# Performance work log

Measured on AMD Instinct MI355X. Metric: run time of the kernel, lower is better.

The kernel has to match this reference:

```python
import jax, jax.numpy as jnp
import numpy as np

B, S, H, NH = 4, 2048, 1024, 16
HD = H // NH
SCALE = 1.0 / np.sqrt(HD)
MASK_VAL = -1e9  # fp32 branch of the torch code


def setup_inputs() -> dict:
    key = jax.random.key(0)
    ks = jax.random.split(key, 6)
    s = 1.0 / np.sqrt(H)
    return {
        "x": jax.random.normal(ks[0], (B, S, H), dtype=jnp.float32),
        "attention_mask": jnp.ones((B, S), dtype=jnp.int32),
        "Wq": jax.random.normal(ks[1], (H, H), dtype=jnp.float32) * s,
        "Wk": jax.random.normal(ks[2], (H, H), dtype=jnp.float32) * s,
        "Wv": jax.random.normal(ks[3], (H, H), dtype=jnp.float32) * s,
        "Wo": jax.random.normal(ks[4], (H, H), dtype=jnp.float32) * s,
        "bo": jnp.zeros((H,), dtype=jnp.float32),
    }


def reference(x, attention_mask, Wq, Wk, Wv, Wo, bo):
    b, s, h = x.shape
    # projections; torch Linear computes x @ W.T
    q = (x @ Wq.T).reshape(b, s, NH, HD).transpose(0, 2, 1, 3)  # [b,nh,s,hd]
    k = (x @ Wk.T).reshape(b, s, NH, HD).transpose(0, 2, 1, 3)
    v = (x @ Wv.T).reshape(b, s, NH, HD).transpose(0, 2, 1, 3)

    scores = jnp.einsum("bhqd,bhkd->bhqk", q, k) * SCALE  # [b,nh,s,s]
    # padding mask: [b,1,1,s]
    pad = (attention_mask == 0)[:, None, None, :]
    scores = jnp.where(pad, MASK_VAL, scores)
    # causal mask
    causal = jnp.tril(jnp.ones((s, s), dtype=bool))[None, None]
    scores = jnp.where(causal, scores, MASK_VAL)

    attn = jax.nn.softmax(scores, axis=-1)  # dropout p=0 / eval -> identity
    out = jnp.einsum("bhqk,bhkd->bhqd", attn, v)
    out = out.transpose(0, 2, 1, 3).reshape(b, s, h)
    return out @ Wo.T + bo
```

## Files before the change

kernel.cpp:

```cpp
#include <hip/hip_runtime.h>

#define B_ 4
#define S_ 2048
#define H_ 1024
#define NH_ 16
#define HD_ 64
#define QSCALE_ 0.1803368801111204f

typedef __attribute__((ext_vector_type(8))) short bf16x8;
typedef __attribute__((ext_vector_type(4))) float f32x4;
typedef __attribute__((ext_vector_type(16))) float f32x16;

__device__ __forceinline__ unsigned short f2bf(float f) {
    unsigned u = __float_as_uint(f);
    unsigned r = (u + 0x7FFFu + ((u >> 16) & 1u)) >> 16;
    return (unsigned short)r;
}
__device__ __forceinline__ float exp2f_hw(float x) { return __builtin_amdgcn_exp2f(x); }

__global__ __launch_bounds__(256) void cast_all(const float* __restrict__ x,
                                                const float* __restrict__ Wq,
                                                const float* __restrict__ Wk,
                                                const float* __restrict__ Wv,
                                                const float* __restrict__ Wo,
                                                unsigned short* __restrict__ xb,
                                                unsigned short* __restrict__ Wqb,
                                                unsigned short* __restrict__ Wkb,
                                                unsigned short* __restrict__ Wvb,
                                                unsigned short* __restrict__ Wob) {
    int bid = blockIdx.x;
    const float* src;
    unsigned short* dst;
    int i;
    if (bid < 8192) {
        src = x; dst = xb; i = bid * 256 + threadIdx.x;
    } else {
        int k = bid - 8192, wsel = k >> 10;
        src = wsel == 0 ? Wq : wsel == 1 ? Wk : wsel == 2 ? Wv : Wo;
        dst = wsel == 0 ? Wqb : wsel == 1 ? Wkb : wsel == 2 ? Wvb : Wob;
        i = (k & 1023) * 256 + threadIdx.x;
    }
    float4 v = reinterpret_cast<const float4*>(src)[i];
    ushort4 o;
    o.x = f2bf(v.x); o.y = f2bf(v.y); o.z = f2bf(v.z); o.w = f2bf(v.w);
    reinterpret_cast<ushort4*>(dst)[i] = o;
}

__device__ __forceinline__ void stage128_swz(const char* g, int gstride, char* lds, int tid) {
    int wave = tid >> 6, lane = tid & 63;
#pragma unroll
    for (int j = 0; j < 4; ++j) {
        int o = ((wave * 4 + j) * 64 + lane) * 16;
        int r = o >> 7;
        int slot = (o >> 4) & 7;
        const char* src = g + (size_t)r * gstride + ((slot ^ (r & 7)) << 4);
        __builtin_amdgcn_global_load_lds((const __attribute__((address_space(1))) void*)src,
                                         (__attribute__((address_space(3))) void*)(lds + (wave * 4 + j) * 1024),
                                         16, 0, 0);
    }
}
__device__ __forceinline__ void stage64_swz(const char* g, int gstride, char* lds, int tid) {
    int wave = tid >> 6, lane = tid & 63;
#pragma unroll
    for (int j = 0; j < 2; ++j) {
        int o = ((wave * 2 + j) * 64 + lane) * 16;
        int r = o >> 7;
        int slot = (o >> 4) & 7;
        const char* src = g + (size_t)r * gstride + ((slot ^ (r & 7)) << 4);
        __builtin_amdgcn_global_load_lds((const __attribute__((address_space(1))) void*)src,
                                         (__attribute__((address_space(3))) void*)(lds + (wave * 2 + j) * 1024),
                                         16, 0, 0);
    }
}

__device__ __forceinline__ bf16x8 frag_swz(const char* lds, int row, int slot) {
    return *reinterpret_cast<const bf16x8*>(lds + row * 128 + (((slot) ^ (row & 7)) << 4));
}

__device__ __forceinline__ float vmax16(const f32x16& v) {
    float a0 = fmaxf(v[0], v[1]), a1 = fmaxf(v[2], v[3]);
    float a2 = fmaxf(v[4], v[5]), a3 = fmaxf(v[6], v[7]);
    float a4 = fmaxf(v[8], v[9]), a5 = fmaxf(v[10], v[11]);
    float a6 = fmaxf(v[12], v[13]), a7 = fmaxf(v[14], v[15]);
    float b0 = fmaxf(a0, a1), b1 = fmaxf(a2, a3), b2 = fmaxf(a4, a5), b3 = fmaxf(a6, a7);
    return fmaxf(fmaxf(b0, b1), fmaxf(b2, b3));
}

__global__ __launch_bounds__(256) void gemm_qkv(const unsigned short* __restrict__ xb,
                                                const unsigned short* __restrict__ Wq,
                                                const unsigned short* __restrict__ Wk,
                                                const unsigned short* __restrict__ Wv,
                                                unsigned short* __restrict__ Qo,
                                                unsigned short* __restrict__ Ko,
                                                unsigned short* __restrict__ Vo) {
    __shared__ __align__(16) char As[128 * 128];
    __shared__ __align__(16) char Bs[128 * 128];
    int tid = threadIdx.x, lane = tid & 63, wave = tid >> 6;
    int wr = wave >> 1, wc = wave & 1;
    int brow = blockIdx.x * 128;
    int mat = blockIdx.y >> 3;
    int bcol = (blockIdx.y & 7) * 128;
    const unsigned short* W = mat == 0 ? Wq : (mat == 1 ? Wk : Wv);
    unsigned short* O = mat == 0 ? Qo : (mat == 1 ? Ko : Vo);
    float oscale = (mat == 0) ? QSCALE_ : 1.0f;
    f32x4 acc[4][4] = {};
    const char* ga = (const char*)(xb + (size_t)brow * H_);
    const char* gb = (const char*)(W + (size_t)bcol * H_);
    int ro = lane & 15, kg = lane >> 4;
    for (int kt = 0; kt < H_ / 64; ++kt) {
        stage128_swz(ga + kt * 128, H_ * 2, As, tid);
        stage128_swz(gb + kt * 128, H_ * 2, Bs, tid);
        __syncthreads();
#pragma unroll
        for (int kk = 0; kk < 2; ++kk) {
            bf16x8 af[4], bfr[4];
#pragma unroll
            for (int m = 0; m < 4; ++m) af[m] = frag_swz(As, wr * 64 + m * 16 + ro, kk * 4 + kg);
#pragma unroll
            for (int n = 0; n < 4; ++n) bfr[n] = frag_swz(Bs, wc * 64 + n * 16 + ro, kk * 4 + kg);
#pragma unroll
            for (int m = 0; m < 4; ++m)
#pragma unroll
                for (int n = 0; n < 4; ++n)
                    acc[m][n] = __builtin_amdgcn_mfma_f32_16x16x32_bf16(af[m], bfr[n], acc[m][n], 0, 0, 0);
        }
        __syncthreads();
    }
#pragma unroll
    for (int m = 0; m < 4; ++m)
#pragma unroll
        for (int n = 0; n < 4; ++n)
#pragma unroll
            for (int i = 0; i < 4; ++i) {
                int row = brow + wr * 64 + m * 16 + kg * 4 + i;
                int col = bcol + wc * 64 + n * 16 + ro;
                O[(size_t)row * H_ + col] = f2bf(acc[m][n][i] * oscale);
            }
}

__global__ __launch_bounds__(256) void gemm_out(const unsigned short* __restrict__ Ab,
                                                const unsigned short* __restrict__ Wo,
                                                const float* __restrict__ bo,
                                                float* __restrict__ out) {
    __shared__ __align__(16) char As[128 * 128];
    __shared__ __align__(16) char Bs[128 * 128];
    int tid = threadIdx.x, lane = tid & 63, wave = tid >> 6;
    int wr = wave >> 1, wc = wave & 1;
    int brow = blockIdx.x * 128;
    int bcol = blockIdx.y * 128;
    f32x4 acc[4][4] = {};
    const char* ga = (const char*)(Ab + (size_t)brow * H_);
    const char* gb = (const char*)(Wo + (size_t)bcol * H_);
    int ro = lane & 15, kg = lane >> 4;
    for (int kt = 0; kt < H_ / 64; ++kt) {
        stage128_swz(ga + kt * 128, H_ * 2, As, tid);
        stage128_swz(gb + kt * 128, H_ * 2, Bs, tid);
        __syncthreads();
#pragma unroll
        for (int kk = 0; kk < 2; ++kk) {
            bf16x8 af[4], bfr[4];
#pragma unroll
            for (int m = 0; m < 4; ++m) af[m] = frag_swz(As, wr * 64 + m * 16 + ro, kk * 4 + kg);
#pragma unroll
            for (int n = 0; n < 4; ++n) bfr[n] = frag_swz(Bs, wc * 64 + n * 16 + ro, kk * 4 + kg);
#pragma unroll
            for (int m = 0; m < 4; ++m)
#pragma unroll
                for (int n = 0; n < 4; ++n)
                    acc[m][n] = __builtin_amdgcn_mfma_f32_16x16x32_bf16(af[m], bfr[n], acc[m][n], 0, 0, 0);
        }
        __syncthreads();
    }
#pragma unroll
    for (int n = 0; n < 4; ++n) {
        int col = bcol + wc * 64 + n * 16 + ro;
        float bn = bo[col];
#pragma unroll
        for (int m = 0; m < 4; ++m)
#pragma unroll
            for (int i = 0; i < 4; ++i) {
                int row = brow + wr * 64 + m * 16 + kg * 4 + i;
                out[(size_t)row * H_ + col] = acc[m][n][i] + bn;
            }
    }
}

__global__ __launch_bounds__(256) void attn(const unsigned short* __restrict__ Q,
                                            const unsigned short* __restrict__ K,
                                            const unsigned short* __restrict__ V,
                                            const int* __restrict__ amask,
                                            unsigned short* __restrict__ Ab) {
    __shared__ __align__(16) char Ksm[2 * 64 * 128];
    __shared__ __align__(16) unsigned short Vt[64 * 64];
    __shared__ unsigned char maskc[2048];
    __shared__ unsigned char anyz[32];

    int tid = threadIdx.x, lane = tid & 63, w = tid >> 6;
    int l31 = lane & 31, hi = lane >> 5, hi4 = hi * 4;
    int id = blockIdx.x;
    int qb = 15 - (id >> 6);
    int bh = id & 63, b = bh >> 4, h = bh & 15;
    int brow = qb * 128;
    int Qwg = brow + w * 32;

    unsigned cm = 0;
#pragma unroll
    for (int r = 0; r < 16; ++r)
        if (((r & 3) + 8 * (r >> 2) + hi4) > l31) cm |= (1u << r);

    const unsigned short* Qg = Q + (size_t)(b * S_ + Qwg + l31) * H_ + h * HD_;
    const unsigned short* Kg = K + (size_t)b * S_ * H_ + h * HD_;
    const unsigned short* Vg = V + (size_t)b * S_ * H_ + h * HD_;

    stage64_swz((const char*)Kg, H_ * 2, Ksm, tid);
    bf16x8 vreg[2];
#pragma unroll
    for (int c = 0; c < 2; ++c) {
        int cid = c * 256 + tid;
        int r = cid & 63, d0 = (cid >> 6) * 8;
        vreg[c] = *reinterpret_cast<const bf16x8*>(Vg + (size_t)r * H_ + d0);
    }
    {
        const int4* am4 = reinterpret_cast<const int4*>(amask + b * S_);
        for (int i = tid; i < S_ / 4; i += 256) {
            int4 v = am4[i];
            uchar4 o;
            o.x = (v.x == 0); o.y = (v.y == 0); o.z = (v.z == 0); o.w = (v.w == 0);
            reinterpret_cast<uchar4*>(maskc)[i] = o;
        }
    }
    bf16x8 qf[4];
#pragma unroll
    for (int kk = 0; kk < 4; ++kk)
        qf[kk] = *reinterpret_cast<const bf16x8*>(Qg + kk * 16 + hi * 8);

    __syncthreads();
    if (tid < 32) {
        const unsigned* mw = reinterpret_cast<const unsigned*>(maskc + tid * 64);
        unsigned o = 0;
#pragma unroll
        for (int i = 0; i < 16; ++i) o |= mw[i];
        anyz[tid] = o ? 1 : 0;
    }

    f32x16 oacc0, oacc1;
#pragma unroll
    for (int j = 0; j < 16; ++j) { oacc0[j] = 0.f; oacc1[j] = 0.f; }
    float mrun = -__builtin_inff(), lrun = 0.f;

    int T = 2 * qb + 2;
    for (int t = 0; t < T; ++t) {
        int kv0 = t * 64;
        const char* Kc = Ksm + (t & 1) * 8192;

#pragma unroll
        for (int c = 0; c < 2; ++c) {
            int cid = c * 256 + tid;
            int r = cid & 63, d0 = (cid >> 6) * 8;
            unsigned short* vb = Vt + d0 * 64 + (r & 7);
            int rs3 = (r >> 3) << 3;
#pragma unroll
            for (int j = 0; j < 8; ++j)
                vb[j * 64 + (rs3 ^ (j << 3))] = (unsigned short)vreg[c][j];
        }
        __syncthreads();

        if (t + 1 < T)
            stage64_swz((const char*)(Kg + (size_t)(kv0 + 64) * H_), H_ * 2,
                        Ksm + ((t + 1) & 1) * 8192, tid);
        {
            int kvn = (t + 1 < T) ? kv0 + 64 : kv0;
#pragma unroll
            for (int c = 0; c < 2; ++c) {
                int cid = c * 256 + tid;
                int r = cid & 63, d0 = (cid >> 6) * 8;
                vreg[c] = *reinterpret_cast<const bf16x8*>(Vg + (size_t)(kvn + r) * H_ + d0);
            }
        }

        int c0 = kv0, c1 = kv0 + 32;
        if (c0 <= Qwg) {
            bool vis1 = (c1 <= Qwg);
            f32x16 sa0, sa1;
#pragma unroll
            for (int j = 0; j < 16; ++j) { sa0[j] = 0.f; sa1[j] = 0.f; }

            __builtin_amdgcn_s_setprio(1);
#pragma unroll
            for (int kk = 0; kk < 4; ++kk) {
                bf16x8 kf0 = frag_swz(Kc, l31, 2 * kk + hi);
                sa0 = __builtin_amdgcn_mfma_f32_32x32x16_bf16(kf0, qf[kk], sa0, 0, 0, 0);
                if (vis1) {
                    bf16x8 kf1 = frag_swz(Kc, 32 + l31, 2 * kk + hi);
                    sa1 = __builtin_amdgcn_mfma_f32_32x32x16_bf16(kf1, qf[kk], sa1, 0, 0, 0);
                }
            }
            __builtin_amdgcn_s_setprio(0);

            if (c0 == Qwg) {
#pragma unroll
                for (int r = 0; r < 16; ++r) sa0[r] = (cm & (1u << r)) ? -1e9f : sa0[r];
            }
            if (vis1 && c1 == Qwg) {
#pragma unroll
                for (int r = 0; r < 16; ++r) sa1[r] = (cm & (1u << r)) ? -1e9f : sa1[r];
            }
            if (anyz[t]) {
#pragma unroll
                for (int u = 0; u < 4; ++u) {
                    uchar4 mk = *reinterpret_cast<const uchar4*>(maskc + kv0 + 8 * u + hi4);
                    if (mk.x) sa0[4 * u + 0] = -1e9f;
                    if (mk.y) sa0[4 * u + 1] = -1e9f;
                    if (mk.z) sa0[4 * u + 2] = -1e9f;
                    if (mk.w) sa0[4 * u + 3] = -1e9f;
                }
                if (vis1) {
#pragma unroll
                    for (int u = 0; u < 4; ++u) {
                        uchar4 mk = *reinterpret_cast<const uchar4*>(maskc + kv0 + 32 + 8 * u + hi4);
                        if (mk.x) sa1[4 * u + 0] = -1e9f;
                        if (mk.y) sa1[4 * u + 1] = -1e9f;
                        if (mk.z) sa1[4 * u + 2] = -1e9f;
                        if (mk.w) sa1[4 * u + 3] = -1e9f;
                    }
                }
            }

            float mx = vmax16(sa0);
            if (vis1) mx = fmaxf(mx, vmax16(sa1));
            mx = fmaxf(mx, __shfl_xor(mx, 32));

            if (__any(mx > mrun + 10.f)) {
                float mnew = fmaxf(mrun, mx);
                float fsc = exp2f_hw(mrun - mnew);
                mrun = mnew;
                lrun *= fsc;
#pragma unroll
                for (int j = 0; j < 16; ++j) { oacc0[j] *= fsc; oacc1[j] *= fsc; }
            }

            float rs = 0.f;
            __builtin_amdgcn_s_setprio(1);
#pragma unroll
            for (int n = 0; n < 2; ++n) {
                if (n == 1 && !vis1) break;
                const f32x16& sa = (n == 0) ? sa0 : sa1;
                unsigned int wrd[4][2];
#pragma unroll
                for (int u = 0; u < 4; ++u) {
                    float p0 = exp2f_hw(sa[4 * u + 0] - mrun);
                    float p1 = exp2f_hw(sa[4 * u + 1] - mrun);
                    float p2 = exp2f_hw(sa[4 * u + 2] - mrun);
                    float p3 = exp2f_hw(sa[4 * u + 3] - mrun);
                    rs += (p0 + p1) + (p2 + p3);
                    asm("v_cvt_pk_bf16_f32 %0, %1, %2" : "=v"(wrd[u][0]) : "v"(p0), "v"(p1));
                    asm("v_cvt_pk_bf16_f32 %0, %1, %2" : "=v"(wrd[u][1]) : "v"(p2), "v"(p3));
                }
#pragma unroll
                for (int half = 0; half < 2; ++half) {
                    int u0 = 2 * half;
                    unsigned int X0 = wrd[u0][0], Y0 = wrd[u0 + 1][0];
                    unsigned int X1 = wrd[u0][1], Y1 = wrd[u0 + 1][1];
                    asm("v_permlane32_swap_b32 %0, %1" : "+v"(X0), "+v"(Y0));
                    asm("v_permlane32_swap_b32 %0, %1" : "+v"(X1), "+v"(Y1));
                    union { unsigned int u[4]; bf16x8 v; } bu;
                    bu.u[0] = X0; bu.u[1] = X1; bu.u[2] = Y0; bu.u[3] = Y1;
                    int kc = 2 * n + half;
                    bf16x8 af0 = *reinterpret_cast<const bf16x8*>(
                        &Vt[(l31) * 64 + (((2 * kc + hi) ^ (l31 & 7)) << 3)]);
                    oacc0 = __builtin_amdgcn_mfma_f32_32x32x16_bf16(af0, bu.v, oacc0, 0, 0, 0);
                    bf16x8 af1 = *reinterpret_cast<const bf16x8*>(
                        &Vt[(32 + l31) * 64 + (((2 * kc + hi) ^ (l31 & 7)) << 3)]);
                    oacc1 = __builtin_amdgcn_mfma_f32_32x32x16_bf16(af1, bu.v, oacc1, 0, 0, 0);
                }
            }
            __builtin_amdgcn_s_setprio(0);

            rs += __shfl_xor(rs, 32);
            lrun += rs;
        }
        __syncthreads();
    }

    float inv = 1.f / lrun;
    unsigned short* Osm = reinterpret_cast<unsigned short*>(Ksm);
#pragma unroll
    for (int r = 0; r < 16; ++r) {
        int d = (r & 3) + 8 * (r >> 2) + hi4;
        Osm[w * 2048 + l31 * 64 + ((((d >> 3) ^ (l31 & 7)) << 3) | (d & 7))] = f2bf(oacc0[r] * inv);
        int d1 = d + 32;
        Osm[w * 2048 + l31 * 64 + ((((d1 >> 3) ^ (l31 & 7)) << 3) | (d1 & 7))] = f2bf(oacc1[r] * inv);
    }
    __syncthreads();
#pragma unroll
    for (int wv = 0; wv < 4; ++wv) {
        int q = tid >> 3, j = tid & 7;
        bf16x8 vv = *reinterpret_cast<const bf16x8*>(Osm + wv * 2048 + q * 64 + ((j ^ (q & 7)) << 3));
        size_t row = (size_t)(b * S_ + brow + wv * 32 + q);
        *reinterpret_cast<bf16x8*>(Ab + row * H_ + h * HD_ + j * 8) = vv;
    }
}

extern "C" void kernel_launch(void* const* d_in, const int* in_sizes, int n_in,
                              void* d_out, int out_size, void* d_ws, size_t ws_size,
                              hipStream_t stream) {
    const float* x  = (const float*)d_in[0];
    const int* amask = (const int*)d_in[1];
    const float* Wq = (const float*)d_in[2];
    const float* Wk = (const float*)d_in[3];
    const float* Wv = (const float*)d_in[4];
    const float* Wo = (const float*)d_in[5];
    const float* bo = (const float*)d_in[6];
    float* out = (float*)d_out;

    const size_t XN = (size_t)B_ * S_ * H_;
    const size_t WN = (size_t)H_ * H_;

    char* ws = (char*)d_ws;
    unsigned short* xb  = (unsigned short*)ws;           ws += XN * 2;
    unsigned short* Wqb = (unsigned short*)ws;           ws += WN * 2;
    unsigned short* Wkb = (unsigned short*)ws;           ws += WN * 2;
    unsigned short* Wvb = (unsigned short*)ws;           ws += WN * 2;
    unsigned short* Wob = (unsigned short*)ws;           ws += WN * 2;
    unsigned short* Qb  = (unsigned short*)ws;           ws += XN * 2;
    unsigned short* Kb  = (unsigned short*)ws;           ws += XN * 2;
    unsigned short* Vb  = (unsigned short*)ws;           ws += XN * 2;
    unsigned short* Ab  = (unsigned short*)ws;           ws += XN * 2;

    cast_all<<<12288, 256, 0, stream>>>(x, Wq, Wk, Wv, Wo, xb, Wqb, Wkb, Wvb, Wob);
    gemm_qkv<<<dim3(64, 24), 256, 0, stream>>>(xb, Wqb, Wkb, Wvb, Qb, Kb, Vb);
    attn<<<1024, 256, 0, stream>>>(Qb, Kb, Vb, amask, Ab);
    gemm_out<<<dim3(64, 8), 256, 0, stream>>>(Ab, Wob, bo, out);
}
```

Baseline: 185.0 us.

## Use 256-row query tiles with 512-thread attention blocks and XCD-aware GEMM block remapping

Attention blocks now cover 256 query rows with 8 waves, so each K/V tile staged in LDS is shared by twice as many query rows. The query-block order is changed to interleave heavy and light causal blocks. The GEMM kernels switch to a 1D grid with a remap that groups tiles by block index modulo 8, likely so that tiles sharing operands land on the same XCD's L2. The trade-off is fewer, larger attention blocks, which means coarser causal load balance and more pressure from 512-thread blocks.

Result: faster. 166.8 us (-9.8%).

```diff
diff --git a/kernel.cpp b/kernel.cpp
--- a/kernel.cpp
+++ b/kernel.cpp
@@ -59,18 +59,15 @@
                                          16, 0, 0);
     }
 }
-__device__ __forceinline__ void stage64_swz(const char* g, int gstride, char* lds, int tid) {
+__device__ __forceinline__ void stage64_swz8(const char* g, int gstride, char* lds, int tid) {
     int wave = tid >> 6, lane = tid & 63;
-#pragma unroll
-    for (int j = 0; j < 2; ++j) {
-        int o = ((wave * 2 + j) * 64 + lane) * 16;
-        int r = o >> 7;
-        int slot = (o >> 4) & 7;
-        const char* src = g + (size_t)r * gstride + ((slot ^ (r & 7)) << 4);
-        __builtin_amdgcn_global_load_lds((const __attribute__((address_space(1))) void*)src,
-                                         (__attribute__((address_space(3))) void*)(lds + (wave * 2 + j) * 1024),
-                                         16, 0, 0);
-    }
+    int o = (wave * 64 + lane) * 16;
+    int r = o >> 7;
+    int slot = (o >> 4) & 7;
+    const char* src = g + (size_t)r * gstride + ((slot ^ (r & 7)) << 4);
+    __builtin_amdgcn_global_load_lds((const __attribute__((address_space(1))) void*)src,
+                                     (__attribute__((address_space(3))) void*)(lds + wave * 1024 + lane * 16),
+                                     16, 0, 0);
 }
 
 __device__ __forceinline__ bf16x8 frag_swz(const char* lds, int row, int slot) {
@@ -97,9 +94,13 @@
     __shared__ __align__(16) char Bs[128 * 128];
     int tid = threadIdx.x, lane = tid & 63, wave = tid >> 6;
     int wr = wave >> 1, wc = wave & 1;
-    int brow = blockIdx.x * 128;
-    int mat = blockIdx.y >> 3;
-    int bcol = (blockIdx.y & 7) * 128;
+    int bid = blockIdx.x;
+    int t = (bid & 7) * 192 + (bid >> 3);
+    int xrow = t / 24;
+    int ym = t - xrow * 24;
+    int brow = xrow * 128;
+    int mat = ym >> 3;
+    int bcol = (ym & 7) * 128;
     const unsigned short* W = mat == 0 ? Wq : (mat == 1 ? Wk : Wv);
     unsigned short* O = mat == 0 ? Qo : (mat == 1 ? Ko : Vo);
     float oscale = (mat == 0) ? QSCALE_ : 1.0f;
@@ -146,8 +147,10 @@
     __shared__ __align__(16) char Bs[128 * 128];
     int tid = threadIdx.x, lane = tid & 63, wave = tid >> 6;
     int wr = wave >> 1, wc = wave & 1;
-    int brow = blockIdx.x * 128;
-    int bcol = blockIdx.y * 128;
+    int bid = blockIdx.x;
+    int t = (bid & 7) * 64 + (bid >> 3);
+    int brow = (t >> 3) * 128;
+    int bcol = (t & 7) * 128;
     f32x4 acc[4][4] = {};
     const char* ga = (const char*)(Ab + (size_t)brow * H_);
     const char* gb = (const char*)(Wo + (size_t)bcol * H_);
@@ -185,22 +188,24 @@
     }
 }
 
-__global__ __launch_bounds__(256) void attn(const unsigned short* __restrict__ Q,
+__global__ __launch_bounds__(512) void attn(const unsigned short* __restrict__ Q,
                                             const unsigned short* __restrict__ K,
                                             const unsigned short* __restrict__ V,
                                             const int* __restrict__ amask,
                                             unsigned short* __restrict__ Ab) {
-    __shared__ __align__(16) char Ksm[2 * 64 * 128];
-    __shared__ __align__(16) unsigned short Vt[64 * 64];
-    __shared__ unsigned char maskc[2048];
-    __shared__ unsigned char anyz[32];
+    __shared__ __align__(16) char lds[32768];
+    char* Ksm = lds;
+    unsigned short* Vt = (unsigned short*)(lds + 16384);
+    unsigned char* maskc = (unsigned char*)(lds + 24576);
+    unsigned char* anyz = (unsigned char*)(lds + 26624);
 
     int tid = threadIdx.x, lane = tid & 63, w = tid >> 6;
     int l31 = lane & 31, hi = lane >> 5, hi4 = hi * 4;
     int id = blockIdx.x;
-    int qb = 15 - (id >> 6);
+    int g = id >> 6;
+    int qb = (g < 4) ? (7 - 2 * g) : (2 * g - 8);
     int bh = id & 63, b = bh >> 4, h = bh & 15;
-    int brow = qb * 128;
+    int brow = qb * 256;
     int Qwg = brow + w * 32;
 
     unsigned cm = 0;
@@ -212,17 +217,13 @@
     const unsigned short* Kg = K + (size_t)b * S_ * H_ + h * HD_;
     const unsigned short* Vg = V + (size_t)b * S_ * H_ + h * HD_;
 
-    stage64_swz((const char*)Kg, H_ * 2, Ksm, tid);
-    bf16x8 vreg[2];
-#pragma unroll
-    for (int c = 0; c < 2; ++c) {
-        int cid = c * 256 + tid;
-        int r = cid & 63, d0 = (cid >> 6) * 8;
-        vreg[c] = *reinterpret_cast<const bf16x8*>(Vg + (size_t)r * H_ + d0);
-    }
+    stage64_swz8((const char*)Kg, H_ * 2, Ksm, tid);
+    int vr = tid & 63, vd0 = (tid >> 6) * 8;
+    bf16x8 vreg = *reinterpret_cast<const bf16x8*>(Vg + (size_t)vr * H_ + vd0);
     {
         const int4* am4 = reinterpret_cast<const int4*>(amask + b * S_);
-        for (int i = tid; i < S_ / 4; i += 256) {
+        int i = tid;
+        if (i < S_ / 4) {
             int4 v = am4[i];
             uchar4 o;
             o.x = (v.x == 0); o.y = (v.y == 0); o.z = (v.z == 0); o.w = (v.w == 0);
@@ -248,34 +249,26 @@
     for (int j = 0; j < 16; ++j) { oacc0[j] = 0.f; oacc1[j] = 0.f; }
     float mrun = -__builtin_inff(), lrun = 0.f;
 
-    int T = 2 * qb + 2;
+    int T = 4 * qb + 4;
     for (int t = 0; t < T; ++t) {
         int kv0 = t * 64;
         const char* Kc = Ksm + (t & 1) * 8192;
 
-#pragma unroll
-        for (int c = 0; c < 2; ++c) {
-            int cid = c * 256 + tid;
-            int r = cid & 63, d0 = (cid >> 6) * 8;
-            unsigned short* vb = Vt + d0 * 64 + (r & 7);
-            int rs3 = (r >> 3) << 3;
+        {
+            unsigned short* vb = Vt + vd0 * 64 + (vr & 7);
+            int rs3 = (vr >> 3) << 3;
 #pragma unroll
             for (int j = 0; j < 8; ++j)
-                vb[j * 64 + (rs3 ^ (j << 3))] = (unsigned short)vreg[c][j];
+                vb[j * 64 + (rs3 ^ (j << 3))] = (unsigned short)vreg[j];
         }
         __syncthreads();
 
         if (t + 1 < T)
-            stage64_swz((const char*)(Kg + (size_t)(kv0 + 64) * H_), H_ * 2,
-                        Ksm + ((t + 1) & 1) * 8192, tid);
+            stage64_swz8((const char*)(Kg + (size_t)(kv0 + 64) * H_), H_ * 2,
+                         Ksm + ((t + 1) & 1) * 8192, tid);
         {
             int kvn = (t + 1 < T) ? kv0 + 64 : kv0;
-#pragma unroll
-            for (int c = 0; c < 2; ++c) {
-                int cid = c * 256 + tid;
-                int r = cid & 63, d0 = (cid >> 6) * 8;
-                vreg[c] = *reinterpret_cast<const bf16x8*>(Vg + (size_t)(kvn + r) * H_ + d0);
-            }
+            vreg = *reinterpret_cast<const bf16x8*>(Vg + (size_t)(kvn + vr) * H_ + vd0);
         }
 
         int c0 = kv0, c1 = kv0 + 32;
@@ -383,7 +376,7 @@
     }
 
     float inv = 1.f / lrun;
-    unsigned short* Osm = reinterpret_cast<unsigned short*>(Ksm);
+    unsigned short* Osm = reinterpret_cast<unsigned short*>(lds);
 #pragma unroll
     for (int r = 0; r < 16; ++r) {
         int d = (r & 3) + 8 * (r >> 2) + hi4;
@@ -395,9 +388,11 @@
 #pragma unroll
     for (int wv = 0; wv < 4; ++wv) {
         int q = tid >> 3, j = tid & 7;
-        bf16x8 vv = *reinterpret_cast<const bf16x8*>(Osm + wv * 2048 + q * 64 + ((j ^ (q & 7)) << 3));
-        size_t row = (size_t)(b * S_ + brow + wv * 32 + q);
-        *reinterpret_cast<bf16x8*>(Ab + row * H_ + h * HD_ + j * 8) = vv;
+        int row = wv * 64 + q;
+        bf16x8 vv = *reinterpret_cast<const bf16x8*>(
+            Osm + (row >> 5) * 2048 + (row & 31) * 64 + ((j ^ (row & 7)) << 3));
+        size_t grow = (size_t)(b * S_ + brow + row);
+        *reinterpret_cast<bf16x8*>(Ab + grow * H_ + h * HD_ + j * 8) = vv;
     }
 }
 
@@ -428,7 +423,7 @@
     unsigned short* Ab  = (unsigned short*)ws;           ws += XN * 2;
 
     cast_all<<<12288, 256, 0, stream>>>(x, Wq, Wk, Wv, Wo, xb, Wqb, Wkb, Wvb, Wob);
-    gemm_qkv<<<dim3(64, 24), 256, 0, stream>>>(xb, Wqb, Wkb, Wvb, Qb, Kb, Vb);
-    attn<<<1024, 256, 0, stream>>>(Qb, Kb, Vb, amask, Ab);
-    gemm_out<<<dim3(64, 8), 256, 0, stream>>>(Ab, Wob, bo, out);
-}
+    gemm_qkv<<<1536, 256, 0, stream>>>(xb, Wqb, Wkb, Wvb, Qb, Kb, Vb);
+    attn<<<512, 512, 0, stream>>>(Qb, Kb, Vb, amask, Ab);
+    gemm_out<<<512, 256, 0, stream>>>(Ab, Wob, bo, out);
+}
```
